# Optimization experiments

Measured on AMD Instinct MI355X. Metric: run time of the kernel, lower is better.

The kernel has to match this reference:

```python
import jax, jax.numpy as jnp
import numpy as np

B, N, D_IN, D_OUT, MAX_POS = 256, 256, 768, 300, 256
NEG_INF = -9e15
LEAKY_SLOPE = 0.2


def setup_inputs() -> dict:
    key = jax.random.key(0)
    ks = jax.random.split(key, 6)
    h = jax.random.normal(ks[0], (B, N, D_IN), dtype=jnp.float32)
    adj = (jax.random.uniform(ks[1], (B, N, N)) > 0.9).astype(jnp.float32)
    adj = jnp.maximum(adj, jnp.eye(N, dtype=jnp.float32)[None])
    positions = jax.random.randint(ks[2], (B, N), 0, MAX_POS)
    W = jax.random.normal(ks[3], (D_IN, D_OUT), dtype=jnp.float32) * (1.0 / np.sqrt(D_IN))
    a_src = jax.random.normal(ks[4], (1, D_OUT), dtype=jnp.float32) * 0.05
    a_dst = jax.random.normal(ks[5], (1, D_OUT), dtype=jnp.float32) * 0.05
    pos_table = jax.random.normal(jax.random.fold_in(key, 7), (MAX_POS, D_OUT), dtype=jnp.float32)
    return {"h": h, "adj": adj, "positions": positions, "W": W,
            "a_src": a_src, "a_dst": a_dst, "pos_table": pos_table}


def reference(h, adj, positions, W, a_src, a_dst, pos_table):
    # Wh = W(h) + position embedding          [B, N, D_OUT]
    Wh = jnp.einsum('bni,io->bno', h, W) + pos_table[positions]
    # additive attention scores
    f_src = jnp.einsum('bno,o->bn', Wh, a_src[0])  # [B, N]
    f_dst = jnp.einsum('bno,o->bn', Wh, a_dst[0])  # [B, N]
    e = f_src[:, :, None] + f_dst[:, None, :]      # [B, N, N]
    e = jnp.where(e >= 0, e, LEAKY_SLOPE * e)      # LeakyReLU(0.2)
    # adjacency masking + softmax over last dim
    masked = jnp.where(adj > 0, e, NEG_INF)
    attention = jax.nn.softmax(masked, axis=-1)
    # (eval mode: edge dropout and dropout are identity)
    h_prime = jnp.einsum('bnm,bmo->bno', attention, Wh)
    return h_prime, attention
```

## Files before the change

kernel.cpp:

```cpp
#include <hip/hip_runtime.h>

#define B_    256
#define N_    256
#define DIN   768
#define DOUT  300
#define DOUTP 304
#define M_    (B_*N_)
#define HP_ELEMS (M_*DOUT)
#define NEG_INF -9.0e15f

typedef _Float16 f16;
typedef __attribute__((ext_vector_type(8))) _Float16 f16x8;
typedef __attribute__((ext_vector_type(4))) _Float16 f16x4;
typedef __attribute__((ext_vector_type(4))) float    f32x4;

__global__ __launch_bounds__(256) void prep_wt(const float* __restrict__ W,
                                               f16* __restrict__ Wt) {
    int idx = blockIdx.x * 256 + threadIdx.x;
    if (idx >= DOUTP * DIN) return;
    int n = idx / DIN, k = idx - n * DIN;
    float v = (n < DOUT) ? W[k * DOUT + n] : 0.0f;
    Wt[idx] = (f16)v;
}

__global__ __launch_bounds__(256, 2) void gemm1(
    const float* __restrict__ h, const f16* __restrict__ Wt,
    const int* __restrict__ positions,
    const float* __restrict__ a_src, const float* __restrict__ a_dst,
    const float* __restrict__ pos_table,
    f16* __restrict__ WhT, float* __restrict__ f_src, float* __restrict__ f_dst)
{
    __shared__ f16 Al[64 * 40];
    __shared__ f16 Bl[DOUTP * 40];

    const int tid  = threadIdx.x;
    const int wave = tid >> 6, lane = tid & 63;
    const int quad = lane >> 4, c = lane & 15;
    const int rowbase = blockIdx.x * 64;

    f32x4 acc[19];
#pragma unroll
    for (int t = 0; t < 19; ++t) acc[t] = (f32x4){0.f, 0.f, 0.f, 0.f};

    for (int kt = 0; kt < DIN / 32; ++kt) {
        {
            int r = tid >> 2, c4 = tid & 3;
            const float4* src = (const float4*)(h + (size_t)(rowbase + r) * DIN + kt * 32);
            float4 v0 = src[c4];
            float4 v1 = src[c4 + 4];
            *(f16x4*)&Al[r * 40 + c4 * 4]      = (f16x4){(f16)v0.x, (f16)v0.y, (f16)v0.z, (f16)v0.w};
            *(f16x4*)&Al[r * 40 + 16 + c4 * 4] = (f16x4){(f16)v1.x, (f16)v1.y, (f16)v1.z, (f16)v1.w};
        }
        for (int i = tid; i < DOUTP * 8; i += 256) {
            int n = i >> 3, j4 = i & 7;
            f16x4 u = *(const f16x4*)(Wt + (size_t)n * DIN + kt * 32 + j4 * 4);
            *(f16x4*)&Bl[n * 40 + j4 * 4] = u;
        }
        __syncthreads();
        f16x8 af = *(const f16x8*)&Al[(wave * 16 + c) * 40 + quad * 8];
#pragma unroll
        for (int t = 0; t < 19; ++t) {
            f16x8 bf = *(const f16x8*)&Bl[(t * 16 + c) * 40 + quad * 8];
            acc[t] = __builtin_amdgcn_mfma_f32_16x16x32_f16(af, bf, acc[t], 0, 0, 0);
        }
        __syncthreads();
    }

    const int grow0 = rowbase + wave * 16 + quad * 4;
    const int bidx  = rowbase >> 8;
    const int mbase = (rowbase & 255) + wave * 16 + quad * 4;

    int pos[4];
#pragma unroll
    for (int r = 0; r < 4; ++r) pos[r] = positions[grow0 + r];

    float fs[4] = {0, 0, 0, 0}, fd[4] = {0, 0, 0, 0};
#pragma unroll
    for (int t = 0; t < 19; ++t) {
        int col = t * 16 + c;
        if (col < DOUT) {
            float as = a_src[col], ad = a_dst[col];
#pragma unroll
            for (int r = 0; r < 4; ++r) {
                float v = acc[t][r] + pos_table[pos[r] * DOUT + col];
                acc[t][r] = v;
                fs[r] += v * as;
                fd[r] += v * ad;
            }
        } else {
#pragma unroll
            for (int r = 0; r < 4; ++r) acc[t][r] = 0.0f;
        }
    }
#pragma unroll
    for (int off = 1; off < 16; off <<= 1) {
#pragma unroll
        for (int r = 0; r < 4; ++r) {
            fs[r] += __shfl_xor(fs[r], off, 16);
            fd[r] += __shfl_xor(fd[r], off, 16);
        }
    }
    if (c == 0) {
        *(float4*)(f_src + grow0) = make_float4(fs[0], fs[1], fs[2], fs[3]);
        *(float4*)(f_dst + grow0) = make_float4(fd[0], fd[1], fd[2], fd[3]);
    }
#pragma unroll
    for (int t = 0; t < 19; ++t) {
        int col = t * 16 + c;
        f16x4 u = (f16x4){(f16)acc[t][0], (f16)acc[t][1], (f16)acc[t][2], (f16)acc[t][3]};
        *(f16x4*)(WhT + ((size_t)bidx * DOUTP + col) * N_ + mbase) = u;
    }
}

__global__ __launch_bounds__(256) void softmax_att(
    const float* __restrict__ adj, const float* __restrict__ f_src,
    const float* __restrict__ f_dst, float* __restrict__ att)
{
    const int wave = threadIdx.x >> 6, lane = threadIdx.x & 63;
    const int row = blockIdx.x * 4 + wave;
    const int b = row >> 8;

    float fs = f_src[row];
    float4 fd4 = *(const float4*)(f_dst + b * N_ + lane * 4);
    float4 a4  = *(const float4*)(adj + (size_t)row * N_ + lane * 4);

    float e[4];
    {
        float v;
        v = fs + fd4.x; v = v >= 0.f ? v : 0.2f * v; e[0] = a4.x > 0.f ? v : NEG_INF;
        v = fs + fd4.y; v = v >= 0.f ? v : 0.2f * v; e[1] = a4.y > 0.f ? v : NEG_INF;
        v = fs + fd4.z; v = v >= 0.f ? v : 0.2f * v; e[2] = a4.z > 0.f ? v : NEG_INF;
        v = fs + fd4.w; v = v >= 0.f ? v : 0.2f * v; e[3] = a4.w > 0.f ? v : NEG_INF;
    }
    float mx = fmaxf(fmaxf(e[0], e[1]), fmaxf(e[2], e[3]));
#pragma unroll
    for (int off = 1; off < 64; off <<= 1) mx = fmaxf(mx, __shfl_xor(mx, off, 64));

    float p[4], s = 0.f;
#pragma unroll
    for (int i = 0; i < 4; ++i) { p[i] = __expf(e[i] - mx); s += p[i]; }
#pragma unroll
    for (int off = 1; off < 64; off <<= 1) s += __shfl_xor(s, off, 64);

    float inv = 1.0f / s;
    *(float4*)(att + (size_t)row * N_ + lane * 4) =
        make_float4(p[0] * inv, p[1] * inv, p[2] * inv, p[3] * inv);
}

__global__ __launch_bounds__(256, 2) void gemm2(
    const float* __restrict__ att, const f16* __restrict__ WhT,
    float* __restrict__ hp)
{
    __shared__ f16 Al[64 * 40];
    __shared__ f16 Bl[DOUTP * 40];

    const int tid  = threadIdx.x;
    const int wave = tid >> 6, lane = tid & 63;
    const int quad = lane >> 4, c = lane & 15;
    const int rowbase = blockIdx.x * 64;
    const int bidx = rowbase >> 8;

    f32x4 acc[19];
#pragma unroll
    for (int t = 0; t < 19; ++t) acc[t] = (f32x4){0.f, 0.f, 0.f, 0.f};

    for (int kt = 0; kt < N_ / 32; ++kt) {
        {
            int r = tid >> 2, c4 = tid & 3;
            const float4* src = (const float4*)(att + (size_t)(rowbase + r) * N_ + kt * 32);
            float4 v0 = src[c4];
            float4 v1 = src[c4 + 4];
            *(f16x4*)&Al[r * 40 + c4 * 4]      = (f16x4){(f16)v0.x, (f16)v0.y, (f16)v0.z, (f16)v0.w};
            *(f16x4*)&Al[r * 40 + 16 + c4 * 4] = (f16x4){(f16)v1.x, (f16)v1.y, (f16)v1.z, (f16)v1.w};
        }
        for (int i = tid; i < DOUTP * 8; i += 256) {
            int n = i >> 3, j4 = i & 7;
            f16x4 u = *(const f16x4*)(WhT + ((size_t)bidx * DOUTP + n) * N_ + kt * 32 + j4 * 4);
            *(f16x4*)&Bl[n * 40 + j4 * 4] = u;
        }
        __syncthreads();
        f16x8 af = *(const f16x8*)&Al[(wave * 16 + c) * 40 + quad * 8];
#pragma unroll
        for (int t = 0; t < 19; ++t) {
            f16x8 bf = *(const f16x8*)&Bl[(t * 16 + c) * 40 + quad * 8];
            acc[t] = __builtin_amdgcn_mfma_f32_16x16x32_f16(af, bf, acc[t], 0, 0, 0);
        }
        __syncthreads();
    }

    const int grow0 = rowbase + wave * 16 + quad * 4;
#pragma unroll
    for (int t = 0; t < 19; ++t) {
        int col = t * 16 + c;
        if (col < DOUT) {
#pragma unroll
            for (int r = 0; r < 4; ++r)
                hp[(size_t)(grow0 + r) * DOUT + col] = acc[t][r];
        }
    }
}

extern "C" void kernel_launch(void* const* d_in, const int* in_sizes, int n_in,
                              void* d_out, int out_size, void* d_ws, size_t ws_size,
                              hipStream_t stream)
{
    const float* h         = (const float*)d_in[0];
    const float* adj       = (const float*)d_in[1];
    const int*   positions = (const int*)d_in[2];
    const float* W         = (const float*)d_in[3];
    const float* a_src     = (const float*)d_in[4];
    const float* a_dst     = (const float*)d_in[5];
    const float* pos_table = (const float*)d_in[6];

    float* hp  = (float*)d_out;
    float* att = hp + HP_ELEMS;

    f16*   Wt    = (f16*)d_ws;
    f16*   WhT   = Wt + (size_t)DOUTP * DIN;
    float* f_src = (float*)(WhT + (size_t)B_ * DOUTP * N_);
    float* f_dst = f_src + M_;

    hipLaunchKernelGGL(prep_wt,     dim3((DOUTP * DIN + 255) / 256), dim3(256), 0, stream, W, Wt);
    hipLaunchKernelGGL(gemm1,       dim3(M_ / 64),  dim3(256), 0, stream,
                       h, Wt, positions, a_src, a_dst, pos_table, WhT, f_src, f_dst);
    hipLaunchKernelGGL(softmax_att, dim3(M_ / 4),   dim3(256), 0, stream, adj, f_src, f_dst, att);
    hipLaunchKernelGGL(gemm2,       dim3(M_ / 64),  dim3(256), 0, stream, att, WhT, hp);
}
```

Before: 548.6 us.

## Use async global-to-LDS loads with swizzled B tiles and 2x2 wave tiling in GEMMs

```diff
diff --git a/kernel.cpp b/kernel.cpp
--- a/kernel.cpp
+++ b/kernel.cpp
@@ -4,7 +4,8 @@
 #define N_    256
 #define DIN   768
 #define DOUT  300
-#define DOUTP 304
+#define DOUTP 320
+#define NT    20
 #define M_    (B_*N_)
 #define HP_ELEMS (M_*DOUT)
 #define NEG_INF -9.0e15f
@@ -13,6 +14,12 @@
 typedef __attribute__((ext_vector_type(8))) _Float16 f16x8;
 typedef __attribute__((ext_vector_type(4))) _Float16 f16x4;
 typedef __attribute__((ext_vector_type(4))) float    f32x4;
+
+__device__ __forceinline__ void async_copy16(void* lds, const void* g) {
+    __builtin_amdgcn_global_load_lds(
+        (const __attribute__((address_space(1))) void*)g,
+        (__attribute__((address_space(3))) void*)lds, 16, 0, 0);
+}
 
 __global__ __launch_bounds__(256) void prep_wt(const float* __restrict__ W,
                                                f16* __restrict__ Wt) {
@@ -23,7 +30,7 @@
     Wt[idx] = (f16)v;
 }
 
-__global__ __launch_bounds__(256, 2) void gemm1(
+__global__ __launch_bounds__(256, 3) void gemm1(
     const float* __restrict__ h, const f16* __restrict__ Wt,
     const int* __restrict__ positions,
     const float* __restrict__ a_src, const float* __restrict__ a_dst,
@@ -31,84 +38,123 @@
     f16* __restrict__ WhT, float* __restrict__ f_src, float* __restrict__ f_dst)
 {
     __shared__ f16 Al[64 * 40];
-    __shared__ f16 Bl[DOUTP * 40];
+    __shared__ f16 Bl[DOUTP * 32];
+    __shared__ float pfs[64][2], pfd[64][2];
 
     const int tid  = threadIdx.x;
     const int wave = tid >> 6, lane = tid & 63;
     const int quad = lane >> 4, c = lane & 15;
+    const int rh = wave & 1;
+    const int chf = wave >> 1;
     const int rowbase = blockIdx.x * 64;
 
-    f32x4 acc[19];
-#pragma unroll
-    for (int t = 0; t < 19; ++t) acc[t] = (f32x4){0.f, 0.f, 0.f, 0.f};
+    const int brow = lane >> 2;
+    const int bj   = (lane & 3) ^ (brow & 3);
+
+    const int ar = tid >> 2, aj = tid & 3;
+
+    f32x4 acc[2][10];
+#pragma unroll
+    for (int rt = 0; rt < 2; ++rt)
+#pragma unroll
+        for (int i = 0; i < 10; ++i) acc[rt][i] = (f32x4){0.f, 0.f, 0.f, 0.f};
 
     for (int kt = 0; kt < DIN / 32; ++kt) {
+#pragma unroll
+        for (int i = 0; i < 5; ++i) {
+            int chk = wave + 4 * i;
+            int n = chk * 16 + brow;
+            async_copy16((char*)Bl + chk * 1024,
+                         Wt + (size_t)n * DIN + kt * 32 + bj * 8);
+        }
         {
-            int r = tid >> 2, c4 = tid & 3;
-            const float4* src = (const float4*)(h + (size_t)(rowbase + r) * DIN + kt * 32);
-            float4 v0 = src[c4];
-            float4 v1 = src[c4 + 4];
-            *(f16x4*)&Al[r * 40 + c4 * 4]      = (f16x4){(f16)v0.x, (f16)v0.y, (f16)v0.z, (f16)v0.w};
-            *(f16x4*)&Al[r * 40 + 16 + c4 * 4] = (f16x4){(f16)v1.x, (f16)v1.y, (f16)v1.z, (f16)v1.w};
-        }
-        for (int i = tid; i < DOUTP * 8; i += 256) {
-            int n = i >> 3, j4 = i & 7;
-            f16x4 u = *(const f16x4*)(Wt + (size_t)n * DIN + kt * 32 + j4 * 4);
-            *(f16x4*)&Bl[n * 40 + j4 * 4] = u;
-        }
-        __syncthreads();
-        f16x8 af = *(const f16x8*)&Al[(wave * 16 + c) * 40 + quad * 8];
-#pragma unroll
-        for (int t = 0; t < 19; ++t) {
-            f16x8 bf = *(const f16x8*)&Bl[(t * 16 + c) * 40 + quad * 8];
-            acc[t] = __builtin_amdgcn_mfma_f32_16x16x32_f16(af, bf, acc[t], 0, 0, 0);
-        }
-        __syncthreads();
-    }
-
-    const int grow0 = rowbase + wave * 16 + quad * 4;
+            const float4* src = (const float4*)(h + (size_t)(rowbase + ar) * DIN + kt * 32 + aj * 8);
+            float4 v0 = src[0], v1 = src[1];
+            *(f16x8*)&Al[ar * 40 + aj * 8] =
+                (f16x8){(f16)v0.x, (f16)v0.y, (f16)v0.z, (f16)v0.w,
+                        (f16)v1.x, (f16)v1.y, (f16)v1.z, (f16)v1.w};
+        }
+        __syncthreads();
+
+        f16x8 af0 = *(const f16x8*)&Al[(rh * 32 + c) * 40 + quad * 8];
+        f16x8 af1 = *(const f16x8*)&Al[(rh * 32 + 16 + c) * 40 + quad * 8];
+#pragma unroll
+        for (int i = 0; i < 10; ++i) {
+            int n = (chf * 10 + i) * 16 + c;
+            f16x8 bf = *(const f16x8*)&Bl[n * 32 + (quad ^ (n & 3)) * 8];
+            acc[0][i] = __builtin_amdgcn_mfma_f32_16x16x32_f16(af0, bf, acc[0][i], 0, 0, 0);
+            acc[1][i] = __builtin_amdgcn_mfma_f32_16x16x32_f16(af1, bf, acc[1][i], 0, 0, 0);
+        }
+        __syncthreads();
+    }
+
     const int bidx  = rowbase >> 8;
-    const int mbase = (rowbase & 255) + wave * 16 + quad * 4;
-
-    int pos[4];
-#pragma unroll
-    for (int r = 0; r < 4; ++r) pos[r] = positions[grow0 + r];
-
-    float fs[4] = {0, 0, 0, 0}, fd[4] = {0, 0, 0, 0};
-#pragma unroll
-    for (int t = 0; t < 19; ++t) {
-        int col = t * 16 + c;
+    const int mloc  = (rowbase & 255);
+
+    int posr[2][4];
+#pragma unroll
+    for (int rt = 0; rt < 2; ++rt)
+#pragma unroll
+        for (int r = 0; r < 4; ++r)
+            posr[rt][r] = positions[rowbase + rh * 32 + rt * 16 + quad * 4 + r];
+
+    float fs[2][4] = {{0,0,0,0},{0,0,0,0}}, fd[2][4] = {{0,0,0,0},{0,0,0,0}};
+#pragma unroll
+    for (int i = 0; i < 10; ++i) {
+        int col = (chf * 10 + i) * 16 + c;
         if (col < DOUT) {
             float as = a_src[col], ad = a_dst[col];
 #pragma unroll
+            for (int rt = 0; rt < 2; ++rt)
+#pragma unroll
+                for (int r = 0; r < 4; ++r) {
+                    float v = acc[rt][i][r] + pos_table[posr[rt][r] * DOUT + col];
+                    acc[rt][i][r] = v;
+                    fs[rt][r] += v * as;
+                    fd[rt][r] += v * ad;
+                }
+        } else {
+#pragma unroll
+            for (int rt = 0; rt < 2; ++rt)
+#pragma unroll
+                for (int r = 0; r < 4; ++r) acc[rt][i][r] = 0.0f;
+        }
+    }
+#pragma unroll
+    for (int off = 1; off < 16; off <<= 1) {
+#pragma unroll
+        for (int rt = 0; rt < 2; ++rt)
+#pragma unroll
             for (int r = 0; r < 4; ++r) {
-                float v = acc[t][r] + pos_table[pos[r] * DOUT + col];
-                acc[t][r] = v;
-                fs[r] += v * as;
-                fd[r] += v * ad;
+                fs[rt][r] += __shfl_xor(fs[rt][r], off, 16);
+                fd[rt][r] += __shfl_xor(fd[rt][r], off, 16);
             }
-        } else {
-#pragma unroll
-            for (int r = 0; r < 4; ++r) acc[t][r] = 0.0f;
-        }
-    }
-#pragma unroll
-    for (int off = 1; off < 16; off <<= 1) {
-#pragma unroll
-        for (int r = 0; r < 4; ++r) {
-            fs[r] += __shfl_xor(fs[r], off, 16);
-            fd[r] += __shfl_xor(fd[r], off, 16);
-        }
     }
     if (c == 0) {
-        *(float4*)(f_src + grow0) = make_float4(fs[0], fs[1], fs[2], fs[3]);
-        *(float4*)(f_dst + grow0) = make_float4(fd[0], fd[1], fd[2], fd[3]);
-    }
-#pragma unroll
-    for (int t = 0; t < 19; ++t) {
-        int col = t * 16 + c;
-        f16x4 u = (f16x4){(f16)acc[t][0], (f16)acc[t][1], (f16)acc[t][2], (f16)acc[t][3]};
-        *(f16x4*)(WhT + ((size_t)bidx * DOUTP + col) * N_ + mbase) = u;
+#pragma unroll
+        for (int rt = 0; rt < 2; ++rt)
+#pragma unroll
+            for (int r = 0; r < 4; ++r) {
+                int row = rh * 32 + rt * 16 + quad * 4 + r;
+                pfs[row][chf] = fs[rt][r];
+                pfd[row][chf] = fd[rt][r];
+            }
+    }
+#pragma unroll
+    for (int i = 0; i < 10; ++i) {
+        int col = (chf * 10 + i) * 16 + c;
+#pragma unroll
+        for (int rt = 0; rt < 2; ++rt) {
+            int mrow = mloc + rh * 32 + rt * 16 + quad * 4;
+            f16x4 u = (f16x4){(f16)acc[rt][i][0], (f16)acc[rt][i][1],
+                              (f16)acc[rt][i][2], (f16)acc[rt][i][3]};
+            *(f16x4*)(WhT + ((size_t)bidx * DOUTP + col) * N_ + mrow) = u;
+        }
+    }
+    __syncthreads();
+    if (tid < 64) {
+        f_src[rowbase + tid] = pfs[tid][0] + pfs[tid][1];
+        f_dst[rowbase + tid] = pfd[tid][0] + pfd[tid][1];
     }
 }
 
@@ -147,55 +193,71 @@
         make_float4(p[0] * inv, p[1] * inv, p[2] * inv, p[3] * inv);
 }
 
-__global__ __launch_bounds__(256, 2) void gemm2(
+__global__ __launch_bounds__(256, 3) void gemm2(
     const float* __restrict__ att, const f16* __restrict__ WhT,
     float* __restrict__ hp)
 {
     __shared__ f16 Al[64 * 40];
-    __shared__ f16 Bl[DOUTP * 40];
+    __shared__ f16 Bl[DOUTP * 32];
 
     const int tid  = threadIdx.x;
     const int wave = tid >> 6, lane = tid & 63;
     const int quad = lane >> 4, c = lane & 15;
+    const int rh = wave & 1;
+    const int chf = wave >> 1;
     const int rowbase = blockIdx.x * 64;
     const int bidx = rowbase >> 8;
 
-    f32x4 acc[19];
-#pragma unroll
-    for (int t = 0; t < 19; ++t) acc[t] = (f32x4){0.f, 0.f, 0.f, 0.f};
+    const int brow = lane >> 2;
+    const int bj   = (lane & 3) ^ (brow & 3);
+    const int ar = tid >> 2, aj = tid & 3;
+
+    f32x4 acc[2][10];
+#pragma unroll
+    for (int rt = 0; rt < 2; ++rt)
+#pragma unroll
+        for (int i = 0; i < 10; ++i) acc[rt][i] = (f32x4){0.f, 0.f, 0.f, 0.f};
 
     for (int kt = 0; kt < N_ / 32; ++kt) {
+#pragma unroll
+        for (int i = 0; i < 5; ++i) {
+            int chk = wave + 4 * i;
+            int n = chk * 16 + brow;
+            async_copy16((char*)Bl + chk * 1024,
+                         WhT + ((size_t)bidx * DOUTP + n) * N_ + kt * 32 + bj * 8);
+        }
         {
-            int r = tid >> 2, c4 = tid & 3;
-            const float4* src = (const float4*)(att + (size_t)(rowbase + r) * N_ + kt * 32);
-            float4 v0 = src[c4];
-            float4 v1 = src[c4 + 4];
-            *(f16x4*)&Al[r * 40 + c4 * 4]      = (f16x4){(f16)v0.x, (f16)v0.y, (f16)v0.z, (f16)v0.w};
-            *(f16x4*)&Al[r * 40 + 16 + c4 * 4] = (f16x4){(f16)v1.x, (f16)v1.y, (f16)v1.z, (f16)v1.w};
-        }
-        for (int i = tid; i < DOUTP * 8; i += 256) {
-            int n = i >> 3, j4 = i & 7;
-            f16x4 u = *(const f16x4*)(WhT + ((size_t)bidx * DOUTP + n) * N_ + kt * 32 + j4 * 4);
-            *(f16x4*)&Bl[n * 40 + j4 * 4] = u;
-        }
-        __syncthreads();
-        f16x8 af = *(const f16x8*)&Al[(wave * 16 + c) * 40 + quad * 8];
-#pragma unroll
-        for (int t = 0; t < 19; ++t) {
-            f16x8 bf = *(const f16x8*)&Bl[(t * 16 + c) * 40 + quad * 8];
-            acc[t] = __builtin_amdgcn_mfma_f32_16x16x32_f16(af, bf, acc[t], 0, 0, 0);
-        }
-        __syncthreads();
-    }
-
-    const int grow0 = rowbase + wave * 16 + quad * 4;
-#pragma unroll
-    for (int t = 0; t < 19; ++t) {
-        int col = t * 16 + c;
+            const float4* src = (const float4*)(att + (size_t)(rowbase + ar) * N_ + kt * 32 + aj * 8);
+            float4 v0 = src[0], v1 = src[1];
+            *(f16x8*)&Al[ar * 40 + aj * 8] =
+                (f16x8){(f16)v0.x, (f16)v0.y, (f16)v0.z, (f16)v0.w,
+                        (f16)v1.x, (f16)v1.y, (f16)v1.z, (f16)v1.w};
+        }
+        __syncthreads();
+
+        f16x8 af0 = *(const f16x8*)&Al[(rh * 32 + c) * 40 + quad * 8];
+        f16x8 af1 = *(const f16x8*)&Al[(rh * 32 + 16 + c) * 40 + quad * 8];
+#pragma unroll
+        for (int i = 0; i < 10; ++i) {
+            int n = (chf * 10 + i) * 16 + c;
+            f16x8 bf = *(const f16x8*)&Bl[n * 32 + (quad ^ (n & 3)) * 8];
+            acc[0][i] = __builtin_amdgcn_mfma_f32_16x16x32_f16(af0, bf, acc[0][i], 0, 0, 0);
+            acc[1][i] = __builtin_amdgcn_mfma_f32_16x16x32_f16(af1, bf, acc[1][i], 0, 0, 0);
+        }
+        __syncthreads();
+    }
+
+#pragma unroll
+    for (int i = 0; i < 10; ++i) {
+        int col = (chf * 10 + i) * 16 + c;
         if (col < DOUT) {
 #pragma unroll
-            for (int r = 0; r < 4; ++r)
-                hp[(size_t)(grow0 + r) * DOUT + col] = acc[t][r];
+            for (int rt = 0; rt < 2; ++rt) {
+                int row0 = rowbase + rh * 32 + rt * 16 + quad * 4;
+#pragma unroll
+                for (int r = 0; r < 4; ++r)
+                    hp[(size_t)(row0 + r) * DOUT + col] = acc[rt][i][r];
+            }
         }
     }
 }
```

After: 471.8 us. 14.0% less time.
